# Kernel optimization log

Hardware: AMD Instinct MI355X
Metric: run time of the kernel (lower is better)

The kernel has to match this reference:

```python
import jax, jax.numpy as jnp
import numpy as np

N = 50000      # nodes
E = 800000     # edges
IN = 256       # input feature dim
H = 3          # num heads (hardcoded in HGAT)
D = 64         # n_hidden = per-head out dim (also n_classes)
EF = 64        # edge_feats
NET = 8        # num edge types
NEG = 0.2      # leaky relu slope
EPS = 1e-12


def setup_inputs() -> dict:
    key = jax.random.key(0)
    ks = jax.random.split(key, 24)
    rn = lambda k, shape: jax.random.normal(k, shape, jnp.float32) * 0.05
    inp = {
        "x": jax.random.normal(ks[0], (N, IN), jnp.float32),
        "src": jax.random.randint(ks[1], (E,), 0, N),
        "dst": jax.random.randint(ks[2], (E,), 0, N),
        "efeat": jax.random.randint(ks[3], (E,), 0, NET),
        # layer 1: in_feats -> n_hidden*H, no residual
        "W1": rn(ks[4], (IN, H * D)),
        "Eemb1": rn(ks[5], (NET, EF)),
        "We1": rn(ks[6], (EF, H * EF)),
        "al1": rn(ks[7], (H, D)),
        "ar1": rn(ks[8], (H, D)),
        "ae1": rn(ks[9], (H, EF)),
        # layer 2: (n_hidden*H) -> n_classes*H, with residual fc
        "W2": rn(ks[10], (H * D, H * D)),
        "Eemb2": rn(ks[11], (NET, EF)),
        "We2": rn(ks[12], (EF, H * EF)),
        "al2": rn(ks[13], (H, D)),
        "ar2": rn(ks[14], (H, D)),
        "ae2": rn(ks[15], (H, EF)),
        "Wres2": rn(ks[16], (H * D, H * D)),
    }
    return inp


def gat_layer(h, src, dst, efeat, W, Eemb, We, al, ar, ae, Wres):
    n = h.shape[0]
    feat = (h @ W).reshape(n, H, -1)                     # [N,H,D]
    e = (Eemb[efeat] @ We).reshape(-1, H, EF)            # [E,H,EF]
    ee = jnp.einsum("ehf,hf->eh", e, ae)                 # [E,H]
    el = jnp.einsum("nhd,hd->nh", feat, al)              # [N,H]
    er = jnp.einsum("nhd,hd->nh", feat, ar)
    logit = jax.nn.leaky_relu(el[src] + er[dst] + ee, NEG)  # [E,H]
    # numerically-stable edge softmax over destination nodes
    mx = jax.ops.segment_max(logit, dst, num_segments=n)
    mx = jnp.where(jnp.isfinite(mx), mx, 0.0)            # zero-in-degree guard
    a = jnp.exp(logit - mx[dst])
    den = jax.ops.segment_sum(a, dst, num_segments=n)
    a = a / jnp.maximum(den[dst], EPS)                   # [E,H]
    rst = jax.ops.segment_sum(a[:, :, None] * feat[src], dst, num_segments=n)  # [N,H,D]
    if Wres is not None:
        rst = rst + (h @ Wres).reshape(n, H, -1)
    return jax.nn.elu(rst)


def reference(x, src, dst, efeat, W1, Eemb1, We1, al1, ar1, ae1,
              W2, Eemb2, We2, al2, ar2, ae2, Wres2):
    h = gat_layer(x, src, dst, efeat, W1, Eemb1, We1, al1, ar1, ae1, None)
    h = h.reshape(N, H * D)  # flatten(1) between layers
    h = gat_layer(h, src, dst, efeat, W2, Eemb2, We2, al2, ar2, ae2, Wres2)
    logits = h.mean(1)       # mean over heads -> [N, n_classes]
    nrm = jnp.linalg.norm(logits, axis=1, keepdims=True)
    return logits / jnp.maximum(nrm, EPS)
```

## Files before the change

### kernel.cpp

```cpp
#include <hip/hip_runtime.h>
#include <cstdint>
#include <cstddef>

#define NN   50000
#define EEN  800000
#define INF_ 256
#define HH   3
#define FEAT 192
#define EFD  64
#define NEG_ 0.2f
#define EPSF 1e-12f
#define SMASK 0x0FFFFFF0
#define NBK  49
#define BKSTR 20480
#define CHUNK 3125

typedef __attribute__((ext_vector_type(8))) short short8;
typedef __attribute__((ext_vector_type(4))) float f32x4;
typedef __attribute__((ext_vector_type(2))) float f32x2;

static __device__ __forceinline__ float4 ld4(const float* p) {
    return *reinterpret_cast<const float4*>(p);
}
static __device__ __forceinline__ uint f2b(float f) {
    union { float f; uint32_t u; } v; v.f = f;
    uint32_t u = v.u;
    return (u + 0x7FFFu + ((u >> 16) & 1u)) >> 16;
}
static __device__ __forceinline__ uint pack2(float a, float b) {
    return f2b(a) | (f2b(b) << 16);
}
static __device__ __forceinline__ float blo(uint u) {
    return __uint_as_float(u << 16);
}
static __device__ __forceinline__ float bhi(uint u) {
    return __uint_as_float(u & 0xFFFF0000u);
}

static __device__ __forceinline__ void trans_tile(const float* __restrict__ W,
        ushort* __restrict__ BT, int K, int N, int kt, int nt)
{
    __shared__ float tile[32][33];
    const int tx = threadIdx.x & 31, ty = threadIdx.x >> 5;
    #pragma unroll
    for (int r = 0; r < 4; ++r) {
        int row = kt * 32 + ty + r * 8;
        int col = nt * 32 + tx;
        tile[ty + r * 8][tx] = W[(size_t)row * N + col];
    }
    __syncthreads();
    #pragma unroll
    for (int r = 0; r < 4; ++r) {
        int n = nt * 32 + ty + r * 8;
        int k = kt * 32 + tx;
        BT[(size_t)n * K + k] = (ushort)f2b(tile[tx][ty + r * 8]);
    }
}

static __device__ __forceinline__ void eetab_calc(const float* __restrict__ Eemb,
        const float* __restrict__ We, const float* __restrict__ ae,
        float* __restrict__ eetab)
{
    __shared__ float t1[3 * 64];
    const int t = threadIdx.x;
    if (t < 192) {
        const int g = t & 63, h = t >> 6;
        const float* wrow = We + g * FEAT + h * EFD;
        const float* av   = ae + h * EFD;
        float s = 0.f;
        #pragma unroll 8
        for (int f = 0; f < EFD; ++f) s += wrow[f] * av[f];
        t1[h * 64 + g] = s;
    }
    __syncthreads();
    if (t < 24) {
        int tt = t / 3, hh = t - tt * 3;
        float acc = 0.f;
        const float* em = Eemb + tt * EFD;
        const float* tv = t1 + hh * 64;
        #pragma unroll 8
        for (int g2 = 0; g2 < 64; ++g2) acc += em[g2] * tv[g2];
        eetab[tt * 3 + hh] = acc;
    }
}

__global__ __launch_bounds__(256) void k_prep(const float* __restrict__ W1,
        ushort* __restrict__ o1, const float* __restrict__ W2,
        ushort* __restrict__ o2, const float* __restrict__ W3,
        ushort* __restrict__ o3,
        const float* __restrict__ Eemb1, const float* __restrict__ We1,
        const float* __restrict__ ae1, float* __restrict__ ee1,
        const float* __restrict__ Eemb2, const float* __restrict__ We2,
        const float* __restrict__ ae2, float* __restrict__ ee2)
{
    int b = blockIdx.x;
    if (b < 48) {
        trans_tile(W1, o1, INF_, FEAT, b & 7, b >> 3);
    } else if (b < 84) {
        int i = b - 48;
        trans_tile(W2, o2, FEAT, FEAT, i % 6, i / 6);
    } else if (b < 120) {
        int i = b - 84;
        trans_tile(W3, o3, FEAT, FEAT, i % 6, i / 6);
    } else if (b == 120) {
        eetab_calc(Eemb1, We1, ae1, ee1);
    } else {
        eetab_calc(Eemb2, We2, ae2, ee2);
    }
}

#define LDA 40
__global__ __launch_bounds__(256) void gemm_mfma1(const float* __restrict__ A,
        const ushort* __restrict__ BT, ushort* __restrict__ Cb,
        float4* __restrict__ el4, float4* __restrict__ er4,
        const float* __restrict__ al, const float* __restrict__ ar,
        int M, int K)
{
    __shared__ ushort As[128 * LDA];
    __shared__ ushort Bs[192 * LDA];
    const int t = threadIdx.x;
    const int lane = t & 63, w = t >> 6;
    const int bm = blockIdx.x * 128;
    const int fr = lane & 15;
    const int fq = lane >> 4;
    const int fg = fq * 8;
    const int arow = t >> 1;
    const int acol = (t & 1) * 8;
    const int brow = t >> 2;
    const int bcol = (t & 3) * 8;

    f32x4 acc[2][12];
    #pragma unroll
    for (int i = 0; i < 2; ++i)
        #pragma unroll
        for (int c = 0; c < 12; ++c)
            acc[i][c] = (f32x4){0.f, 0.f, 0.f, 0.f};

    const int ga = bm + arow;
    for (int k0 = 0; k0 < K; k0 += 32) {
        uint4 u0 = make_uint4(0,0,0,0), u1 = u0;
        if (ga < M) {
            const float* ap = A + (size_t)ga * K + k0 + acol;
            float4 f0 = ld4(ap), f1 = ld4(ap + 4);
            float4 f2v = ld4(ap + 16), f3 = ld4(ap + 20);
            u0 = make_uint4(pack2(f0.x,f0.y), pack2(f0.z,f0.w),
                            pack2(f1.x,f1.y), pack2(f1.z,f1.w));
            u1 = make_uint4(pack2(f2v.x,f2v.y), pack2(f2v.z,f2v.w),
                            pack2(f3.x,f3.y), pack2(f3.z,f3.w));
        }
        *reinterpret_cast<uint4*>(As + arow * LDA + acol) = u0;
        *reinterpret_cast<uint4*>(As + arow * LDA + acol + 16) = u1;
        #pragma unroll
        for (int j = 0; j < 3; ++j) {
            uint4 bv = *reinterpret_cast<const uint4*>(BT + (size_t)(j * 64 + brow) * K + k0 + bcol);
            *reinterpret_cast<uint4*>(Bs + (j * 64 + brow) * LDA + bcol) = bv;
        }
        __syncthreads();
        short8 afr0 = *reinterpret_cast<const short8*>(As + (w * 32 + fr) * LDA + fg);
        short8 afr1 = *reinterpret_cast<const short8*>(As + (w * 32 + 16 + fr) * LDA + fg);
        #pragma unroll
        for (int c = 0; c < 12; ++c) {
            short8 bfr = *reinterpret_cast<const short8*>(Bs + (c * 16 + fr) * LDA + fg);
            acc[0][c] = __builtin_amdgcn_mfma_f32_16x16x32_bf16(afr0, bfr, acc[0][c], 0, 0, 0);
            acc[1][c] = __builtin_amdgcn_mfma_f32_16x16x32_bf16(afr1, bfr, acc[1][c], 0, 0, 0);
        }
        __syncthreads();
    }
    #pragma unroll
    for (int i = 0; i < 2; ++i) {
        #pragma unroll
        for (int j = 0; j < 4; ++j) {
            int row = bm + w * 32 + i * 16 + fq * 4 + j;
            if (row < M) {
                #pragma unroll
                for (int c = 0; c < 12; ++c)
                    Cb[(size_t)row * FEAT + c * 16 + fr] = (ushort)f2b(acc[i][c][j]);
            }
        }
    }
    float alv[12], arv[12];
    #pragma unroll
    for (int c = 0; c < 12; ++c) {
        alv[c] = al[c * 16 + fr];
        arv[c] = ar[c * 16 + fr];
    }
    #pragma unroll
    for (int i = 0; i < 2; ++i) {
        #pragma unroll
        for (int j = 0; j < 4; ++j) {
            int row = bm + w * 32 + i * 16 + fq * 4 + j;
            float pl0 = 0.f, pl1 = 0.f, pl2 = 0.f;
            float pr0 = 0.f, pr1 = 0.f, pr2 = 0.f;
            #pragma unroll
            for (int c = 0; c < 4; ++c)  { pl0 += acc[i][c][j]*alv[c];  pr0 += acc[i][c][j]*arv[c]; }
            #pragma unroll
            for (int c = 4; c < 8; ++c)  { pl1 += acc[i][c][j]*alv[c];  pr1 += acc[i][c][j]*arv[c]; }
            #pragma unroll
            for (int c = 8; c < 12; ++c) { pl2 += acc[i][c][j]*alv[c];  pr2 += acc[i][c][j]*arv[c]; }
            #pragma unroll
            for (int o = 1; o < 16; o <<= 1) {
                pl0 += __shfl_xor(pl0, o); pl1 += __shfl_xor(pl1, o); pl2 += __shfl_xor(pl2, o);
                pr0 += __shfl_xor(pr0, o); pr1 += __shfl_xor(pr1, o); pr2 += __shfl_xor(pr2, o);
            }
            if (fr == 0 && row < M) {
                el4[row] = make_float4(pl0, pl1, pl2, 0.f);
                er4[row] = make_float4(pr0, pr1, pr2, 0.f);
            }
        }
    }
}

__global__ __launch_bounds__(256) void gemm_mfma2(const ushort* __restrict__ A,
        const ushort* __restrict__ BT, const ushort* __restrict__ BT2,
        ushort* __restrict__ Cb, ushort* __restrict__ resb,
        float4* __restrict__ el4, float4* __restrict__ er4,
        const float* __restrict__ al, const float* __restrict__ ar,
        int M, int K)
{
    __shared__ ushort As[64 * LDA];
    __shared__ ushort Bs[192 * LDA];
    __shared__ ushort Bs2[192 * LDA];
    const int t = threadIdx.x;
    const int lane = t & 63, w = t >> 6;
    const int bm = blockIdx.x * 64;
    const int fr = lane & 15;
    const int fq = lane >> 4;
    const int fg = fq * 8;
    const int arow = t >> 2;
    const int acol = (t & 3) * 8;
    const int brow = t >> 2;
    const int bcol = (t & 3) * 8;

    f32x4 acc[12], acc2[12];
    #pragma unroll
    for (int c = 0; c < 12; ++c) {
        acc[c] = (f32x4){0.f, 0.f, 0.f, 0.f};
        acc2[c] = (f32x4){0.f, 0.f, 0.f, 0.f};
    }

    const int ga = bm + arow;
    for (int k0 = 0; k0 < K; k0 += 32) {
        uint4 u0 = make_uint4(0,0,0,0);
        if (ga < M)
            u0 = *reinterpret_cast<const uint4*>(A + (size_t)ga * K + k0 + acol);
        *reinterpret_cast<uint4*>(As + arow * LDA + acol) = u0;
        #pragma unroll
        for (int j = 0; j < 3; ++j) {
            uint4 bv = *reinterpret_cast<const uint4*>(BT + (size_t)(j * 64 + brow) * K + k0 + bcol);
            *reinterpret_cast<uint4*>(Bs + (j * 64 + brow) * LDA + bcol) = bv;
            uint4 b2 = *reinterpret_cast<const uint4*>(BT2 + (size_t)(j * 64 + brow) * K + k0 + bcol);
            *reinterpret_cast<uint4*>(Bs2 + (j * 64 + brow) * LDA + bcol) = b2;
        }
        __syncthreads();
        short8 afr = *reinterpret_cast<const short8*>(As + (w * 16 + fr) * LDA + fg);
        #pragma unroll
        for (int c = 0; c < 12; ++c) {
            short8 bfr = *reinterpret_cast<const short8*>(Bs + (c * 16 + fr) * LDA + fg);
            acc[c] = __builtin_amdgcn_mfma_f32_16x16x32_bf16(afr, bfr, acc[c], 0, 0, 0);
            short8 b2 = *reinterpret_cast<const short8*>(Bs2 + (c * 16 + fr) * LDA + fg);
            acc2[c] = __builtin_amdgcn_mfma_f32_16x16x32_bf16(afr, b2, acc2[c], 0, 0, 0);
        }
        __syncthreads();
    }
    #pragma unroll
    for (int j = 0; j < 4; ++j) {
        int row = bm + w * 16 + fq * 4 + j;
        if (row < M) {
            #pragma unroll
            for (int c = 0; c < 12; ++c) {
                Cb[(size_t)row * FEAT + c * 16 + fr] = (ushort)f2b(acc[c][j]);
                resb[(size_t)row * FEAT + c * 16 + fr] = (ushort)f2b(acc2[c][j]);
            }
        }
    }
    float alv[12], arv[12];
    #pragma unroll
    for (int c = 0; c < 12; ++c) {
        alv[c] = al[c * 16 + fr];
        arv[c] = ar[c * 16 + fr];
    }
    #pragma unroll
    for (int j = 0; j < 4; ++j) {
        int row = bm + w * 16 + fq * 4 + j;
        float pl0 = 0.f, pl1 = 0.f, pl2 = 0.f;
        float pr0 = 0.f, pr1 = 0.f, pr2 = 0.f;
        #pragma unroll
        for (int c = 0; c < 4; ++c)  { pl0 += acc[c][j]*alv[c];  pr0 += acc[c][j]*arv[c]; }
        #pragma unroll
        for (int c = 4; c < 8; ++c)  { pl1 += acc[c][j]*alv[c];  pr1 += acc[c][j]*arv[c]; }
        #pragma unroll
        for (int c = 8; c < 12; ++c) { pl2 += acc[c][j]*alv[c];  pr2 += acc[c][j]*arv[c]; }
        #pragma unroll
        for (int o = 1; o < 16; o <<= 1) {
            pl0 += __shfl_xor(pl0, o); pl1 += __shfl_xor(pl1, o); pl2 += __shfl_xor(pl2, o);
            pr0 += __shfl_xor(pr0, o); pr1 += __shfl_xor(pr1, o); pr2 += __shfl_xor(pr2, o);
        }
        if (fr == 0 && row < M) {
            el4[row] = make_float4(pl0, pl1, pl2, 0.f);
            er4[row] = make_float4(pr0, pr1, pr2, 0.f);
        }
    }
}

__global__ __launch_bounds__(256) void k_bucketA(const int* __restrict__ src,
        const int* __restrict__ dst, const int* __restrict__ et,
        int* __restrict__ bcnt, uint* __restrict__ bko)
{
    __shared__ uint recs[CHUNK];
    __shared__ ushort abk[CHUNK];
    __shared__ int hcnt[NBK], hoff[NBK], hcur[NBK], gb[NBK];
    const int t = threadIdx.x;
    const int e0 = blockIdx.x * CHUNK;
    if (t < NBK) hcnt[t] = 0;
    __syncthreads();
    uint rec[13];
    int  bk[13];
    #pragma unroll
    for (int k = 0; k < 13; ++k) {
        int i = t + k * 256;
        if (i < CHUNK) {
            int e = e0 + i;
            int s = src[e], d = dst[e], tt = et[e];
            rec[k] = (uint)s | ((uint)tt << 16) | ((uint)(d & 1023) << 19);
            bk[k] = d >> 10;
            atomicAdd(&hcnt[bk[k]], 1);
        } else {
            bk[k] = -1;
        }
    }
    __syncthreads();
    if (t < 64) {
        int v = (t < NBK) ? hcnt[t] : 0;
        int incl = v;
        #pragma unroll
        for (int o = 1; o < 64; o <<= 1) {
            int u = __shfl_up(incl, o);
            if (t >= o) incl += u;
        }
        if (t < NBK) { hoff[t] = incl - v; hcur[t] = incl - v; }
    }
    __syncthreads();
    #pragma unroll
    for (int k = 0; k < 13; ++k) {
        if (bk[k] >= 0) {
            int p = atomicAdd(&hcur[bk[k]], 1);
            recs[p] = rec[k];
            abk[p] = (ushort)bk[k];
        }
    }
    __syncthreads();
    if (t < NBK) gb[t] = atomicAdd(&bcnt[t], hcnt[t]);
    __syncthreads();
    for (int i = t; i < CHUNK; i += 256) {
        int b = abk[i];
        bko[(size_t)b * BKSTR + gb[b] + (i - hoff[b])] = recs[i];
    }
}

__global__ __launch_bounds__(64) void k_scanB(const int* __restrict__ bcnt,
        int* __restrict__ bexc, int* __restrict__ off)
{
    int t = threadIdx.x;
    int v = (t < NBK) ? bcnt[t] : 0;
    int incl = v;
    #pragma unroll
    for (int o = 1; o < 64; o <<= 1) {
        int u = __shfl_up(incl, o);
        if (t >= o) incl += u;
    }
    if (t < NBK) bexc[t] = incl - v;
    if (t == 63) off[NN] = incl;
}

__global__ __launch_bounds__(256) void k_bucketB(const int* __restrict__ bcnt,
        const int* __restrict__ bexc, const uint* __restrict__ bko,
        int* __restrict__ off, int* __restrict__ srcP)
{
    __shared__ int ldeg[1024], loff[1024];
    __shared__ int wsum[4];
    const int t = threadIdx.x, b = blockIdx.x;
    const int nd0 = b << 10;
    const int ncnt = min(1024, NN - nd0);
    const int ecnt = bcnt[b];
    const int base = bexc[b];
    const uint* rp = bko + (size_t)b * BKSTR;
    for (int i = t; i < 1024; i += 256) ldeg[i] = 0;
    __syncthreads();
    for (int i = t; i < ecnt; i += 256)
        atomicAdd(&ldeg[rp[i] >> 19], 1);
    __syncthreads();
    {
        int a0 = ldeg[4*t], a1 = ldeg[4*t+1], a2 = ldeg[4*t+2], a3 = ldeg[4*t+3];
        int s = a0 + a1 + a2 + a3;
        int incl = s;
        const int lane = t & 63;
        #pragma unroll
        for (int o = 1; o < 64; o <<= 1) {
            int u = __shfl_up(incl, o);
            if (lane >= o) incl += u;
        }
        int wid = t >> 6;
        if (lane == 63) wsum[wid] = incl;
        __syncthreads();
        int wb = 0;
        #pragma unroll
        for (int q = 0; q < 4; ++q) if (q < wid) wb += wsum[q];
        int tb = wb + incl - s;
        loff[4*t] = tb; loff[4*t+1] = tb + a0;
        loff[4*t+2] = tb + a0 + a1; loff[4*t+3] = tb + a0 + a1 + a2;
    }
    __syncthreads();
    for (int i = t; i < ncnt; i += 256) off[nd0 + i] = base + loff[i];
    for (int i = t; i < 1024; i += 256) ldeg[i] = loff[i];
    __syncthreads();
    for (int i = t; i < ecnt; i += 256) {
        uint rec = rp[i];
        int ld = rec >> 19;
        int p = base + atomicAdd(&ldeg[ld], 1);
        srcP[p] = (int)(((rec & 0xFFFFu) << 4) | (((rec >> 16) & 7u) << 28));
    }
}

#define EXTRACT(U, V01, V23) \
    f32x2 V01 = {blo((U).x), bhi((U).x)}; \
    f32x2 V23 = {blo((U).y), bhi((U).y)};

#define GBODY(WV) { \
    int bo = __float_as_int((WV).w); \
    uint2 x0 = *reinterpret_cast<const uint2*>(fb + bo); \
    uint2 x1 = *reinterpret_cast<const uint2*>(fb + bo + 128); \
    uint2 x2 = *reinterpret_cast<const uint2*>(fb + bo + 256); \
    EXTRACT(x0, v00, v01) \
    EXTRACT(x1, v10, v11) \
    EXTRACT(x2, v20, v21) \
    a00 += (WV).x * v00; a01 += (WV).x * v01; \
    a10 += (WV).y * v10; a11 += (WV).y * v11; \
    a20 += (WV).z * v20; a21 += (WV).z * v21; }

template<bool RES, bool FINAL>
__global__ __launch_bounds__(256) void k_attn_agg(const int* __restrict__ off,
        const int* __restrict__ srcP, const float4* __restrict__ el4,
        const float4* __restrict__ er4, const float* __restrict__ eetab,
        const ushort* __restrict__ featb, const ushort* __restrict__ resb,
        void* __restrict__ outv)
{
    __shared__ float shw[4][4][17][4];
    __shared__ float eet[24];
    const int w = threadIdx.x >> 6, lane = threadIdx.x & 63;
    const int g = lane >> 4, gl = lane & 15;
    if (threadIdx.x < 24) eet[threadIdx.x] = eetab[threadIdx.x];
    __syncthreads();
    const int bid = blockIdx.x;
    const int xcd = bid & 7, bix = bid >> 3;
    const int wg = (xcd < 5 ? xcd * 391 : 5 * 391 + (xcd - 5) * 390) + bix;
    const int n = wg * 16 + w * 4 + g;
    const int beg = off[n], end = off[n + 1];
    const int deg = end - beg;
    int degmax = max(deg, __shfl_xor(deg, 16));
    degmax = max(degmax, __shfl_xor(degmax, 32));
    const float4 erv = er4[n];
    const char* elc = (const char*)el4;
    const char* fb  = (const char*)featb + gl * 8;
    float* slot = &shw[w][g][gl][0];
    const float* sg = &shw[w][g][0][0];

    f32x2 a00 = {0.f,0.f}, a01 = {0.f,0.f};
    f32x2 a10 = {0.f,0.f}, a11 = {0.f,0.f};
    f32x2 a20 = {0.f,0.f}, a21 = {0.f,0.f};
    float dl0 = 0.f, dl1 = 0.f, dl2 = 0.f;

    bool vld = gl < deg;
    int sp = vld ? srcP[beg + gl] : 0;
    float4 ev = vld ? *reinterpret_cast<const float4*>(elc + (sp & SMASK))
                    : make_float4(0.f, 0.f, 0.f, 0.f);

    for (int c0 = 0; c0 < degmax; c0 += 16) {
        float p0 = 0.f, p1 = 0.f, p2 = 0.f;
        int boff = 0;
        if (vld) {
            int s16 = sp & SMASK;
            int tt = ((unsigned)sp) >> 28;
            float l0 = ev.x + erv.x + eet[tt*3+0];
            float l1 = ev.y + erv.y + eet[tt*3+1];
            float l2 = ev.z + erv.z + eet[tt*3+2];
            l0 = l0 > 0.f ? l0 : NEG_ * l0;
            l1 = l1 > 0.f ? l1 : NEG_ * l1;
            l2 = l2 > 0.f ? l2 : NEG_ * l2;
            p0 = __expf(l0); p1 = __expf(l1); p2 = __expf(l2);
            boff = s16 * 24;
        }
        dl0 += p0; dl1 += p1; dl2 += p2;
        *reinterpret_cast<float4*>(slot) = make_float4(p0, p1, p2, __int_as_float(boff));
        int cnt = deg - c0;
        cnt = cnt < 0 ? 0 : (cnt > 16 ? 16 : cnt);
        int cmax = max(cnt, __shfl_xor(cnt, 16));
        cmax = max(cmax, __shfl_xor(cmax, 32));
        const int nc = c0 + 16;
        if (nc < degmax) {
            vld = (nc + gl) < deg;
            sp = vld ? srcP[beg + nc + gl] : 0;
            ev = vld ? *reinterpret_cast<const float4*>(elc + (sp & SMASK))
                     : make_float4(0.f, 0.f, 0.f, 0.f);
        }
        int j = 0;
        for (; j + 4 <= cmax; j += 4) {
            float4 wa = *reinterpret_cast<const float4*>(sg + (j+0)*4);
            float4 wb = *reinterpret_cast<const float4*>(sg + (j+1)*4);
            float4 wc = *reinterpret_cast<const float4*>(sg + (j+2)*4);
            float4 wd = *reinterpret_cast<const float4*>(sg + (j+3)*4);
            GBODY(wa)
            GBODY(wb)
            GBODY(wc)
            GBODY(wd)
        }
        for (; j < cmax; ++j) {
            float4 wa = *reinterpret_cast<const float4*>(sg + j*4);
            GBODY(wa)
        }
    }
    #pragma unroll
    for (int o = 1; o < 16; o <<= 1) {
        dl0 += __shfl_xor(dl0, o);
        dl1 += __shfl_xor(dl1, o);
        dl2 += __shfl_xor(dl2, o);
    }
    const float i0 = 1.f / fmaxf(dl0, EPSF);
    const float i1 = 1.f / fmaxf(dl1, EPSF);
    const float i2 = 1.f / fmaxf(dl2, EPSF);
    float e0 = a00.x*i0, e1 = a00.y*i0, e2 = a01.x*i0, e3 = a01.y*i0;
    float q0 = a10.x*i1, q1 = a10.y*i1, q2 = a11.x*i1, q3 = a11.y*i1;
    float r0 = a20.x*i2, r1 = a20.y*i2, r2 = a21.x*i2, r3 = a21.y*i2;
    if (RES) {
        const char* rb = (const char*)resb + (size_t)n * 384 + gl * 8;
        uint2 u0 = *reinterpret_cast<const uint2*>(rb);
        uint2 u1 = *reinterpret_cast<const uint2*>(rb + 128);
        uint2 u2 = *reinterpret_cast<const uint2*>(rb + 256);
        e0 += blo(u0.x); e1 += bhi(u0.x); e2 += blo(u0.y); e3 += bhi(u0.y);
        q0 += blo(u1.x); q1 += bhi(u1.x); q2 += blo(u1.y); q3 += bhi(u1.y);
        r0 += blo(u2.x); r1 += bhi(u2.x); r2 += blo(u2.y); r3 += bhi(u2.y);
    }
#define ELUF(x) ((x) > 0.f ? (x) : __expf(x) - 1.f)
    e0 = ELUF(e0); e1 = ELUF(e1); e2 = ELUF(e2); e3 = ELUF(e3);
    q0 = ELUF(q0); q1 = ELUF(q1); q2 = ELUF(q2); q3 = ELUF(q3);
    r0 = ELUF(r0); r1 = ELUF(r1); r2 = ELUF(r2); r3 = ELUF(r3);
    if (!FINAL) {
        char* ob = (char*)outv + (size_t)n * 384 + gl * 8;
        *reinterpret_cast<uint2*>(ob)       = make_uint2(pack2(e0,e1), pack2(e2,e3));
        *reinterpret_cast<uint2*>(ob + 128) = make_uint2(pack2(q0,q1), pack2(q2,q3));
        *reinterpret_cast<uint2*>(ob + 256) = make_uint2(pack2(r0,r1), pack2(r2,r3));
    } else {
        float m0 = (e0 + q0 + r0) * (1.f / 3.f);
        float m1 = (e1 + q1 + r1) * (1.f / 3.f);
        float m2 = (e2 + q2 + r2) * (1.f / 3.f);
        float m3 = (e3 + q3 + r3) * (1.f / 3.f);
        float ss = m0*m0 + m1*m1 + m2*m2 + m3*m3;
        #pragma unroll
        for (int o = 1; o < 16; o <<= 1) ss += __shfl_xor(ss, o);
        float invn = 1.f / fmaxf(sqrtf(ss), EPSF);
        *reinterpret_cast<float4*>((float*)outv + (size_t)n * 64 + gl * 4) =
            make_float4(m0 * invn, m1 * invn, m2 * invn, m3 * invn);
    }
}

extern "C" void kernel_launch(void* const* d_in, const int* in_sizes, int n_in,
                              void* d_out, int out_size, void* d_ws, size_t ws_size,
                              hipStream_t stream)
{
    const float* x     = (const float*)d_in[0];
    const int*   src   = (const int*)d_in[1];
    const int*   dst   = (const int*)d_in[2];
    const int*   efeat = (const int*)d_in[3];
    const float* W1    = (const float*)d_in[4];
    const float* Eemb1 = (const float*)d_in[5];
    const float* We1   = (const float*)d_in[6];
    const float* al1   = (const float*)d_in[7];
    const float* ar1   = (const float*)d_in[8];
    const float* ae1   = (const float*)d_in[9];
    const float* W2    = (const float*)d_in[10];
    const float* Eemb2 = (const float*)d_in[11];
    const float* We2   = (const float*)d_in[12];
    const float* al2   = (const float*)d_in[13];
    const float* ar2   = (const float*)d_in[14];
    const float* ae2   = (const float*)d_in[15];
    const float* Wres2 = (const float*)d_in[16];

    char* w = (char*)d_ws;
    auto alloc = [&](size_t bytes) {
        char* p = w;
        w += (bytes + 255) & ~(size_t)255;
        return p;
    };
    ushort* featb = (ushort*)alloc((size_t)NN * FEAT * 2);
    ushort* h1b   = (ushort*)alloc((size_t)NN * FEAT * 2);
    ushort* resb  = (ushort*)alloc((size_t)NN * FEAT * 2);
    float4* el4   = (float4*)alloc((size_t)NN * 16);
    float4* er4   = (float4*)alloc((size_t)NN * 16);
    int*    off   = (int*)alloc((size_t)(NN + 1) * 4);
    int*    srcP  = (int*)alloc((size_t)EEN * 4);
    uint*   bko   = (uint*)alloc((size_t)NBK * BKSTR * 4);
    int*    bcnt  = (int*)alloc(64 * 4);
    int*    bexc  = (int*)alloc(64 * 4);
    ushort* w1bt  = (ushort*)alloc((size_t)FEAT * INF_ * 2);
    ushort* w2bt  = (ushort*)alloc((size_t)FEAT * FEAT * 2);
    ushort* wrbt  = (ushort*)alloc((size_t)FEAT * FEAT * 2);
    float*  ee1   = (float*)alloc(24 * 4);
    float*  ee2   = (float*)alloc(24 * 4);

    hipMemsetAsync(bcnt, 0, 64 * 4, stream);

    k_bucketA<<<EEN / CHUNK, 256, 0, stream>>>(src, dst, efeat, bcnt, bko);
    k_scanB<<<1, 64, 0, stream>>>(bcnt, bexc, off);
    k_bucketB<<<NBK, 256, 0, stream>>>(bcnt, bexc, bko, off, srcP);
    k_prep<<<122, 256, 0, stream>>>(W1, w1bt, W2, w2bt, Wres2, wrbt,
            Eemb1, We1, ae1, ee1, Eemb2, We2, ae2, ee2);

    const int ngb = NN / 16;
    gemm_mfma1<<<(NN + 127) / 128, 256, 0, stream>>>(x, w1bt, featb,
            el4, er4, al1, ar1, NN, INF_);
    k_attn_agg<false, false><<<ngb, 256, 0, stream>>>(off, srcP, el4, er4, ee1,
            featb, nullptr, h1b);
    gemm_mfma2<<<(NN + 63) / 64, 256, 0, stream>>>(h1b, w2bt, wrbt, featb,
            resb, el4, er4, al2, ar2, NN, FEAT);
    k_attn_agg<true, true><<<ngb, 256, 0, stream>>>(off, srcP, el4, er4, ee2,
            featb, resb, (float*)d_out);
}
```

Measured before the change: 210.7 us.

## Sort destination nodes by in-degree to balance attention aggregation waves

Adds a counting sort of nodes by in-degree (histogram, scan, scatter) that builds a permutation. The attention-aggregation kernels then map each 16-lane group to a node taken from this permutation, so nodes sharing a wave have similar degree and degmax-driven loop divergence shrinks. The cost is three extra small kernel launches, one indirection per node, and the loss of the previous XCD-aware contiguous node mapping, which may reduce L2 locality for the output writes.

```diff
diff --git a/kernel.cpp b/kernel.cpp
--- a/kernel.cpp
+++ b/kernel.cpp
@@ -421,6 +421,61 @@
     }
 }
 
+__global__ __launch_bounds__(256) void k_dhist(const int* __restrict__ off,
+        int* __restrict__ dhist)
+{
+    __shared__ int lh[64];
+    const int t = threadIdx.x;
+    if (t < 64) lh[t] = 0;
+    __syncthreads();
+    const int n = blockIdx.x * 256 + t;
+    if (n < NN) {
+        int d = off[n + 1] - off[n];
+        atomicAdd(&lh[min(d, 63)], 1);
+    }
+    __syncthreads();
+    if (t < 64 && lh[t]) atomicAdd(&dhist[t], lh[t]);
+}
+
+__global__ __launch_bounds__(64) void k_dscan(const int* __restrict__ dhist,
+        int* __restrict__ dcur)
+{
+    const int t = threadIdx.x;
+    int v = dhist[t];
+    int incl = v;
+    #pragma unroll
+    for (int o = 1; o < 64; o <<= 1) {
+        int u = __shfl_up(incl, o);
+        if (t >= o) incl += u;
+    }
+    dcur[t] = incl - v;
+}
+
+__global__ __launch_bounds__(256) void k_dscat(const int* __restrict__ off,
+        int* __restrict__ dcur, int* __restrict__ perm)
+{
+    __shared__ int lh[64], lbase[64];
+    const int t = threadIdx.x;
+    if (t < 64) lh[t] = 0;
+    __syncthreads();
+    const int n = blockIdx.x * 256 + t;
+    int bin = -1;
+    if (n < NN) {
+        int d = off[n + 1] - off[n];
+        bin = min(d, 63);
+        atomicAdd(&lh[bin], 1);
+    }
+    __syncthreads();
+    if (t < 64) lbase[t] = lh[t] ? atomicAdd(&dcur[t], lh[t]) : 0;
+    __syncthreads();
+    if (t < 64) lh[t] = 0;
+    __syncthreads();
+    if (n < NN) {
+        int r = atomicAdd(&lh[bin], 1);
+        perm[lbase[bin] + r] = n;
+    }
+}
+
 #define EXTRACT(U, V01, V23) \
     f32x2 V01 = {blo((U).x), bhi((U).x)}; \
     f32x2 V23 = {blo((U).y), bhi((U).y)};
@@ -439,7 +494,8 @@
 
 template<bool RES, bool FINAL>
 __global__ __launch_bounds__(256) void k_attn_agg(const int* __restrict__ off,
-        const int* __restrict__ srcP, const float4* __restrict__ el4,
+        const int* __restrict__ srcP, const int* __restrict__ perm,
+        const float4* __restrict__ el4,
         const float4* __restrict__ er4, const float* __restrict__ eetab,
         const ushort* __restrict__ featb, const ushort* __restrict__ resb,
         void* __restrict__ outv)
@@ -450,10 +506,8 @@
     const int g = lane >> 4, gl = lane & 15;
     if (threadIdx.x < 24) eet[threadIdx.x] = eetab[threadIdx.x];
     __syncthreads();
-    const int bid = blockIdx.x;
-    const int xcd = bid & 7, bix = bid >> 3;
-    const int wg = (xcd < 5 ? xcd * 391 : 5 * 391 + (xcd - 5) * 390) + bix;
-    const int n = wg * 16 + w * 4 + g;
+    const int q = w * 3125 + blockIdx.x;
+    const int n = perm[q * 4 + g];
     const int beg = off[n], end = off[n + 1];
     const int deg = end - beg;
     int degmax = max(deg, __shfl_xor(deg, 16));
@@ -597,30 +651,36 @@
     float4* er4   = (float4*)alloc((size_t)NN * 16);
     int*    off   = (int*)alloc((size_t)(NN + 1) * 4);
     int*    srcP  = (int*)alloc((size_t)EEN * 4);
+    int*    perm  = (int*)alloc((size_t)NN * 4);
     uint*   bko   = (uint*)alloc((size_t)NBK * BKSTR * 4);
     int*    bcnt  = (int*)alloc(64 * 4);
+    int*    dhist = (int*)alloc(64 * 4);
     int*    bexc  = (int*)alloc(64 * 4);
+    int*    dcur  = (int*)alloc(64 * 4);
     ushort* w1bt  = (ushort*)alloc((size_t)FEAT * INF_ * 2);
     ushort* w2bt  = (ushort*)alloc((size_t)FEAT * FEAT * 2);
     ushort* wrbt  = (ushort*)alloc((size_t)FEAT * FEAT * 2);
     float*  ee1   = (float*)alloc(24 * 4);
     float*  ee2   = (float*)alloc(24 * 4);
 
-    hipMemsetAsync(bcnt, 0, 64 * 4, stream);
+    hipMemsetAsync(bcnt, 0, 512, stream);
 
     k_bucketA<<<EEN / CHUNK, 256, 0, stream>>>(src, dst, efeat, bcnt, bko);
     k_scanB<<<1, 64, 0, stream>>>(bcnt, bexc, off);
     k_bucketB<<<NBK, 256, 0, stream>>>(bcnt, bexc, bko, off, srcP);
+    k_dhist<<<196, 256, 0, stream>>>(off, dhist);
+    k_dscan<<<1, 64, 0, stream>>>(dhist, dcur);
+    k_dscat<<<196, 256, 0, stream>>>(off, dcur, perm);
     k_prep<<<122, 256, 0, stream>>>(W1, w1bt, W2, w2bt, Wres2, wrbt,
             Eemb1, We1, ae1, ee1, Eemb2, We2, ae2, ee2);
 
     const int ngb = NN / 16;
     gemm_mfma1<<<(NN + 127) / 128, 256, 0, stream>>>(x, w1bt, featb,
             el4, er4, al1, ar1, NN, INF_);
-    k_attn_agg<false, false><<<ngb, 256, 0, stream>>>(off, srcP, el4, er4, ee1,
-            featb, nullptr, h1b);
+    k_attn_agg<false, false><<<ngb, 256, 0, stream>>>(off, srcP, perm, el4, er4,
+            ee1, featb, nullptr, h1b);
     gemm_mfma2<<<(NN + 63) / 64, 256, 0, stream>>>(h1b, w2bt, wrbt, featb,
             resb, el4, er4, al2, ar2, NN, FEAT);
-    k_attn_agg<true, true><<<ngb, 256, 0, stream>>>(off, srcP, el4, er4, ee2,
-            featb, resb, (float*)d_out);
-}
+    k_attn_agg<true, true><<<ngb, 256, 0, stream>>>(off, srcP, perm, el4, er4,
+            ee2, featb, resb, (float*)d_out);
+}
```

After: 225.3 us. 6.9% more time.
